# Kernel tuning notes

Hardware: AMD Instinct MI355X
Metric: run time of the kernel (lower is better)

Reference implementation:

```python
import math
import jax, jax.numpy as jnp
import numpy as np
from jax import lax

# Fractional-order LIF constants (Teka et al. style fractional LIF)
ALPHA = 0.2          # fractional order (self.frac_order)
DT = 0.1             # ms
V_L = -70.0          # leak reversal
V_RESET = -70.0      # reset potential
V_TH = -50.0         # spike threshold
G_L = 0.025          # leak conductance
CM = 0.5             # membrane capacitance
KAPPA = (DT ** ALPHA) * math.gamma(2.0 - ALPHA)
EXPO = 1.0 - ALPHA


def _flif_scan(I_seq):
    """Fractional LIF over time. I_seq: [T, B, H] -> (spikes, mems) each [T, B, H].
    V_n = KAPPA * (-G_L*(V_{n-1}-V_L) + I_n)/CM + V_{n-1} - memory_n,
    memory_n = sum_{j=1}^{n-1} c_j * dV_{n-1-j},  c_j = (j+1)^{1-a} - j^{1-a}."""
    T, B, H = I_seq.shape
    dt_f = I_seq.dtype
    j = jnp.arange(T + 1, dtype=jnp.float32)
    c = ((j + 1.0) ** EXPO - j ** EXPO).astype(dt_f)  # c[j], valid for j>=1
    ks = jnp.arange(T)

    def step(carry, xs):
        V, hist = carry            # V: [B,H], hist[k] = dV_k: [T,B,H]
        I, n = xs                  # n = 1..T (1-based step index)
        jidx = n - 1 - ks          # lag j for each history slot k
        w = jnp.where(jidx >= 1, c[jnp.clip(jidx, 0, T)], 0.0)
        memory = jnp.einsum('t,tbh->bh', w, hist)
        f = (-G_L * (V - V_L) + I) / CM
        Vn = KAPPA * f + V - memory
        spk = (Vn >= V_TH).astype(dt_f)
        Vr = jnp.where(spk > 0, V_RESET, Vn)
        hist = hist.at[n - 1].set(Vr - V)
        return (Vr, hist), (spk, Vr)

    V0 = jnp.full((B, H), V_RESET, dtype=dt_f)
    hist0 = jnp.zeros((T, B, H), dtype=dt_f)
    _, (spikes, mems) = lax.scan(step, (V0, hist0), (I_seq, jnp.arange(1, T + 1)))
    return spikes, mems


def setup_inputs() -> dict:
    key = jax.random.key(0)
    k1, k2, k3 = jax.random.split(key, 3)
    B, T, NI, NH, NO = 64, 128, 784, 512, 10
    data = jax.random.uniform(k1, (B, T, NI), dtype=jnp.float32)
    kh = 1.0 / np.sqrt(NI)
    W_h = jnp.abs(jax.random.uniform(k2, (NH, NI), minval=-kh, maxval=kh, dtype=jnp.float32) * 6.0)
    ko = 1.0 / np.sqrt(NH)
    W_o = jnp.abs(jax.random.uniform(k3, (NO, NH), minval=-ko, maxval=ko, dtype=jnp.float32) * 5.0)
    return {"data": data, "W_h": W_h, "W_o": W_o}


def reference(data, W_h, W_o):
    # hidden synapses: [B,T,NI] x [NH,NI] -> [T,B,NH] (time-major for scan)
    I_h = jnp.einsum('btn,hn->tbh', data, W_h)
    spk_h, mem_h = _flif_scan(I_h)
    # output synapses applied per step == one GEMM over all steps
    I_o = jnp.einsum('tbh,oh->tbo', spk_h, W_o)
    spk_o, mem_o = _flif_scan(I_o)
    # matches torch.stack(output_spikes_trace), torch.stack(output_values_trace): [T,B,NO]
    return spk_o, mem_o
```

## Files before the change

### kernel.cpp

```cpp
#include <hip/hip_runtime.h>
#include <hip/hip_bf16.h>
#include <cmath>

#define T_STEPS 128
#define BATCH   64
#define NI      784
#define NIP     800
#define NH      512
#define NO      10
#define M1      (T_STEPS*BATCH)
#define NT_H    (BATCH*NH)
#define NT_O    (BATCH*NO)
#define OUT_HALF (T_STEPS*BATCH*NO)
#define TB      8

typedef __attribute__((ext_vector_type(8))) short short8;
typedef __attribute__((ext_vector_type(4))) float f32x4;
typedef __attribute__((ext_vector_type(8))) unsigned short u16x8;

static __device__ __forceinline__ unsigned short f2b_bits(float x) {
    __hip_bfloat16 h = __float2bfloat16(x);
    return *reinterpret_cast<unsigned short*>(&h);
}
static __device__ __forceinline__ float b2f_bits(unsigned short u) {
    union { unsigned int i; float f; } v; v.i = ((unsigned int)u) << 16; return v.f;
}

template <bool FINAL, int STRIDE>
__device__ __forceinline__ void flif_scan_body(const char* __restrict__ inps,
                                               float* __restrict__ hist,
                                               const float* __restrict__ cs,
                                               void* __restrict__ spikes,
                                               float* __restrict__ mems,
                                               int NT, int nid, int li, float kappa) {
    float cn_[TB];
#pragma unroll
    for (int j = 0; j < TB; ++j) cn_[j] = cs[j];

    float V = -70.f;
    unsigned dvbits = 0u;

    for (int t = 0; t < T_STEPS / TB; ++t) {
        const int n0 = t * TB;

        float Ivv[TB];
#pragma unroll
        for (int i = 0; i < TB; ++i) {
            if constexpr (FINAL) Ivv[i] = ((const float*)inps)[(n0 + i) * STRIDE + li];
            else                 Ivv[i] = __bfloat162float(((const __hip_bfloat16*)inps)[(n0 + i) * STRIDE + li]);
        }
        __builtin_amdgcn_sched_barrier(0);

        float old_[TB];
#pragma unroll
        for (int i = 0; i < TB; ++i) old_[i] = 0.f;

        if (__any(dvbits != 0u)) {
            for (int k0 = 0; k0 < n0; k0 += TB) {
                float hv[TB];
                unsigned sb = 0u;
#pragma unroll
                for (int kk = 0; kk < TB; ++kk) {
                    hv[kk] = hist[(k0 + kk) * STRIDE + li];
                    sb |= __float_as_uint(hv[kk]);
                }
                if (__any(sb != 0u)) {
                    const int base = n0 - k0 - (TB - 1);
                    float cw[2 * TB];
#pragma unroll
                    for (int q = 0; q < 4; ++q) {
                        const float4 cv = *reinterpret_cast<const float4*>(cs + (base - 1) + 4 * q);
                        cw[4 * q + 0] = cv.x; cw[4 * q + 1] = cv.y;
                        cw[4 * q + 2] = cv.z; cw[4 * q + 3] = cv.w;
                    }
#pragma unroll
                    for (int kk = 0; kk < TB; ++kk) {
#pragma unroll
                        for (int i = 0; i < TB; ++i)
                            old_[i] += hv[kk] * cw[TB - kk + i];
                    }
                }
            }
        }

        float dvb[TB];
#pragma unroll
        for (int i = 0; i < TB; ++i) {
            const int nm1 = n0 + i;
            const float Iv = Ivv[i];
            const float f  = (-0.025f * (V + 70.f) + Iv) * 2.0f;
            const float Vn = kappa * f + V - old_[i];
            const bool  sp = (Vn >= -50.f);
            const float Vr = sp ? -70.f : Vn;
            const float dv = Vr - V;
            dvb[i] = dv;
            dvbits |= __float_as_uint(dv);
#pragma unroll
            for (int i2 = i + 1; i2 < TB; ++i2)
                old_[i2] += dv * cn_[i2 - i];
            if (FINAL) {
                ((float*)spikes)[(size_t)nm1 * NT + nid] = sp ? 1.f : 0.f;
                mems[(size_t)nm1 * NT + nid] = Vr;
            } else {
                ((__hip_bfloat16*)spikes)[(size_t)nm1 * NT + nid] = __float2bfloat16(sp ? 1.f : 0.f);
            }
            V = Vr;
        }

        __builtin_amdgcn_sched_barrier(0);
#pragma unroll
        for (int i = 0; i < TB; ++i)
            hist[(n0 + i) * STRIDE + li] = dvb[i];
        __builtin_amdgcn_sched_barrier(0);
    }
}

__global__ __launch_bounds__(256) void prep_kernel(const float* __restrict__ data,
                                                   const float* __restrict__ Wh,
                                                   __hip_bfloat16* __restrict__ Ab,
                                                   __hip_bfloat16* __restrict__ Whb,
                                                   float* __restrict__ ctab) {
    const int bid = blockIdx.x;
    if (bid == 0) {
        const int j = threadIdx.x;
        if (j < 192) {
            double a = pow((double)(j + 1), 0.8);
            double b = pow((double)j, 0.8);
            ctab[j] = (float)(a - b);
        }
        return;
    }
    if (bid <= 6400) {
        const int idx = (bid - 1) * 256 + threadIdx.x;
        const int r  = idx / 200;
        const int n4 = (idx - r * 200) * 4;
        ushort4 o;
        if (n4 < NI) {
            const float4 f = *reinterpret_cast<const float4*>(data + (size_t)r * NI + n4);
            o.x = f2b_bits(f.x); o.y = f2b_bits(f.y); o.z = f2b_bits(f.z); o.w = f2b_bits(f.w);
        } else {
            o.x = o.y = o.z = o.w = 0;
        }
        *reinterpret_cast<ushort4*>(Ab + (size_t)r * NIP + n4) = o;
    } else {
        const int idx = (bid - 6401) * 256 + threadIdx.x;
        const int r  = idx / 200;
        const int n4 = (idx - r * 200) * 4;
        ushort4 o;
        if (n4 < NI) {
            const float4 f = *reinterpret_cast<const float4*>(Wh + (size_t)r * NI + n4);
            o.x = f2b_bits(f.x); o.y = f2b_bits(f.y); o.z = f2b_bits(f.z); o.w = f2b_bits(f.w);
        } else {
            o.x = o.y = o.z = o.w = 0;
        }
        *reinterpret_cast<ushort4*>(Whb + (size_t)r * NIP + n4) = o;
    }
}

__global__ __launch_bounds__(256) void fused1_kernel(const __hip_bfloat16* __restrict__ A,
                                                     const __hip_bfloat16* __restrict__ B,
                                                     __hip_bfloat16* __restrict__ Sh,
                                                     const float* __restrict__ ctab,
                                                     float kappa) {
    __shared__ __hip_bfloat16 As[2][128 * 32];
    __shared__ __hip_bfloat16 Bs[2][64 * 32];
    __shared__ __hip_bfloat16 Ibuf[128 * 64];
    __shared__ float          hist[128 * 64];
    __shared__ __attribute__((aligned(16))) float cs[192];

    const int tid  = threadIdx.x;
    const int wave = tid >> 6, lane = tid & 63;
    const int wm = wave >> 1, wn = wave & 1;
    const int b  = blockIdx.x;
    const int hn = blockIdx.y;
    const int lrow = lane >> 2;
    const int lchk = lane & 3;

    const int NTILES = NIP / 32;

    auto STAGE = [&](int buf, int tt) {
        const int k0 = tt * 32;
#pragma unroll
        for (int p = 0; p < 2; ++p) {
            const int rbase = p * 64 + wave * 16;
            const __hip_bfloat16* g = A + (size_t)(b * T_STEPS + rbase + lrow) * NIP + k0 + lchk * 8;
            __builtin_amdgcn_global_load_lds((const __attribute__((address_space(1))) void*)g,
                                             (__attribute__((address_space(3))) void*)(As[buf] + rbase * 32),
                                             16, 0, 0);
        }
        {
            const __hip_bfloat16* g = B + (size_t)(hn * 64 + wave * 16 + lrow) * NIP + k0 + lchk * 8;
            __builtin_amdgcn_global_load_lds((const __attribute__((address_space(1))) void*)g,
                                             (__attribute__((address_space(3))) void*)(Bs[buf] + wave * 16 * 32),
                                             16, 0, 0);
        }
    };

    f32x4 acc[4][2] = {};

    STAGE(0, 0);
    for (int j = tid; j < 192; j += 256) cs[j] = ctab[j];
    __syncthreads();

    int cur = 0;
    for (int t = 0; t < NTILES; ++t) {
        if (t + 1 < NTILES) STAGE(cur ^ 1, t + 1);

        short8 a[4], bb[2];
#pragma unroll
        for (int i = 0; i < 4; ++i)
            a[i] = *reinterpret_cast<const short8*>(As[cur] + (wm * 64 + i * 16 + (lane & 15)) * 32 + (lane >> 4) * 8);
#pragma unroll
        for (int j = 0; j < 2; ++j)
            bb[j] = *reinterpret_cast<const short8*>(Bs[cur] + (wn * 32 + j * 16 + (lane & 15)) * 32 + (lane >> 4) * 8);
#pragma unroll
        for (int i = 0; i < 4; ++i)
#pragma unroll
            for (int j = 0; j < 2; ++j)
                acc[i][j] = __builtin_amdgcn_mfma_f32_16x16x32_bf16(a[i], bb[j], acc[i][j], 0, 0, 0);

        __syncthreads();
        cur ^= 1;
    }

#pragma unroll
    for (int i = 0; i < 4; ++i) {
#pragma unroll
        for (int j = 0; j < 2; ++j) {
            const int col = wn * 32 + j * 16 + (lane & 15);
#pragma unroll
            for (int r2 = 0; r2 < 4; ++r2) {
                const int row = wm * 64 + i * 16 + (lane >> 4) * 4 + r2;
                Ibuf[row * 64 + col] = __float2bfloat16(acc[i][j][r2]);
            }
        }
    }
    __syncthreads();

    if (tid < 64) {
        flif_scan_body<false, 64>((const char*)Ibuf, hist, cs,
                                  (void*)(Sh + (size_t)b * NH), nullptr,
                                  64 * NH, hn * 64 + tid, tid, kappa);
    }
}

__global__ __launch_bounds__(256) void gemm2_kernel(const __hip_bfloat16* __restrict__ S,
                                                    const float* __restrict__ Wo,
                                                    float* __restrict__ Io) {
    const int wave = threadIdx.x >> 6, lane = threadIdx.x & 63;
    const int r0 = (blockIdx.x * 4 + wave) * 4;

    float wreg[NO][8];
#pragma unroll
    for (int o = 0; o < NO; ++o) {
        const float4 w0 = *reinterpret_cast<const float4*>(Wo + (size_t)o * NH + lane * 8);
        const float4 w1 = *reinterpret_cast<const float4*>(Wo + (size_t)o * NH + lane * 8 + 4);
        wreg[o][0] = w0.x; wreg[o][1] = w0.y; wreg[o][2] = w0.z; wreg[o][3] = w0.w;
        wreg[o][4] = w1.x; wreg[o][5] = w1.y; wreg[o][6] = w1.z; wreg[o][7] = w1.w;
    }

#pragma unroll
    for (int rr = 0; rr < 4; ++rr) {
        const int r = r0 + rr;
        u16x8 raw = *reinterpret_cast<const u16x8*>(S + (size_t)r * NH + lane * 8);
        float s[8];
#pragma unroll
        for (int j = 0; j < 8; ++j) s[j] = b2f_bits(raw[j]);
#pragma unroll
        for (int o = 0; o < NO; ++o) {
            float a = 0.f;
#pragma unroll
            for (int j = 0; j < 8; ++j) a += s[j] * wreg[o][j];
#pragma unroll
            for (int off = 32; off; off >>= 1) a += __shfl_xor(a, off);
            if (lane == o) Io[(size_t)r * NO + o] = a;
        }
    }
}

__global__ __launch_bounds__(64) void flif_final_kernel(const float* __restrict__ Io,
                                                        float* __restrict__ spikes,
                                                        float* __restrict__ mems,
                                                        const float* __restrict__ ctab,
                                                        float kappa) {
    __shared__ float hist[T_STEPS * 64];
    __shared__ __attribute__((aligned(16))) float cs[192];
    __shared__ __attribute__((aligned(16))) char inps[T_STEPS * 64 * 4];
    const int lane = threadIdx.x;
    const int nid  = blockIdx.x * 64 + lane;

#pragma unroll
    for (int q = 0; q < 32; ++q) {
        const float* g = Io +
            ((size_t)(q * 4 + (lane >> 4)) * NT_O + (size_t)blockIdx.x * 64 + (lane & 15) * 4);
        __builtin_amdgcn_global_load_lds((const __attribute__((address_space(1))) void*)g,
                                         (__attribute__((address_space(3))) void*)(inps + q * 1024),
                                         16, 0, 0);
    }
    for (int j = lane; j < 192; j += 64) cs[j] = ctab[j];
    __syncthreads();

    flif_scan_body<true, 64>(inps, hist, cs, spikes, mems, NT_O, nid, lane, kappa);
}

extern "C" void kernel_launch(void* const* d_in, const int* in_sizes, int n_in,
                              void* d_out, int out_size, void* d_ws, size_t ws_size,
                              hipStream_t stream) {
    const float* data = (const float*)d_in[0];
    const float* Wh   = (const float*)d_in[1];
    const float* Wo   = (const float*)d_in[2];
    float* out = (float*)d_out;

    char* ws = (char*)d_ws;
    size_t off = 0;
    auto alloc = [&](size_t bytes) { void* p = ws + off; off += (bytes + 255) & ~255ull; return p; };
    __hip_bfloat16* Ab   = (__hip_bfloat16*)alloc((size_t)M1 * NIP * 2);
    __hip_bfloat16* Whb  = (__hip_bfloat16*)alloc((size_t)NH * NIP * 2);
    __hip_bfloat16* Sh   = (__hip_bfloat16*)alloc((size_t)M1 * NH * 2);
    float*          Io   = (float*)alloc((size_t)M1 * NO * 4);
    float*          ctab = (float*)alloc(192 * 4);

    const float kappa = (float)(std::pow(0.1, 0.2) * std::tgamma(1.8));

    prep_kernel<<<6801, 256, 0, stream>>>(data, Wh, Ab, Whb, ctab);

    dim3 g1(BATCH, NH / 64, 1);
    fused1_kernel<<<g1, 256, 0, stream>>>(Ab, Whb, Sh, ctab, kappa);

    gemm2_kernel<<<M1 / 16, 256, 0, stream>>>(Sh, Wo, Io);

    flif_final_kernel<<<NT_O / 64, 64, 0, stream>>>(Io, out, out + OUT_HALF, ctab, kappa);
}
```

Measured before the change: 65.19 us.

## Deepen GEMM load pipeline to four LDS stages with explicit vmcnt waits

```diff
diff --git a/kernel.cpp b/kernel.cpp
--- a/kernel.cpp
+++ b/kernel.cpp
@@ -162,11 +162,12 @@
                                                      __hip_bfloat16* __restrict__ Sh,
                                                      const float* __restrict__ ctab,
                                                      float kappa) {
-    __shared__ __hip_bfloat16 As[2][128 * 32];
-    __shared__ __hip_bfloat16 Bs[2][64 * 32];
-    __shared__ __hip_bfloat16 Ibuf[128 * 64];
-    __shared__ float          hist[128 * 64];
-    __shared__ __attribute__((aligned(16))) float cs[192];
+    __shared__ __attribute__((aligned(16))) char SMEM[66304];
+    __hip_bfloat16* As   = (__hip_bfloat16*)SMEM;
+    __hip_bfloat16* Bs   = (__hip_bfloat16*)(SMEM + 32768);
+    __hip_bfloat16* Ibuf = (__hip_bfloat16*)(SMEM + 49152);
+    float*          hist = (float*)SMEM;
+    float*          cs   = (float*)(SMEM + 65536);
 
     const int tid  = threadIdx.x;
     const int wave = tid >> 6, lane = tid & 63;
@@ -185,13 +186,13 @@
             const int rbase = p * 64 + wave * 16;
             const __hip_bfloat16* g = A + (size_t)(b * T_STEPS + rbase + lrow) * NIP + k0 + lchk * 8;
             __builtin_amdgcn_global_load_lds((const __attribute__((address_space(1))) void*)g,
-                                             (__attribute__((address_space(3))) void*)(As[buf] + rbase * 32),
+                                             (__attribute__((address_space(3))) void*)(As + buf * (128 * 32) + rbase * 32),
                                              16, 0, 0);
         }
         {
             const __hip_bfloat16* g = B + (size_t)(hn * 64 + wave * 16 + lrow) * NIP + k0 + lchk * 8;
             __builtin_amdgcn_global_load_lds((const __attribute__((address_space(1))) void*)g,
-                                             (__attribute__((address_space(3))) void*)(Bs[buf] + wave * 16 * 32),
+                                             (__attribute__((address_space(3))) void*)(Bs + buf * (64 * 32) + wave * 16 * 32),
                                              16, 0, 0);
         }
     };
@@ -199,28 +200,36 @@
     f32x4 acc[4][2] = {};
 
     STAGE(0, 0);
+    STAGE(1, 1);
+    STAGE(2, 2);
     for (int j = tid; j < 192; j += 256) cs[j] = ctab[j];
     __syncthreads();
 
-    int cur = 0;
     for (int t = 0; t < NTILES; ++t) {
-        if (t + 1 < NTILES) STAGE(cur ^ 1, t + 1);
-
+        if (t + 3 < NTILES) STAGE((t + 3) & 3, t + 3);
+
+        const int cur = t & 3;
         short8 a[4], bb[2];
 #pragma unroll
         for (int i = 0; i < 4; ++i)
-            a[i] = *reinterpret_cast<const short8*>(As[cur] + (wm * 64 + i * 16 + (lane & 15)) * 32 + (lane >> 4) * 8);
+            a[i] = *reinterpret_cast<const short8*>(As + cur * (128 * 32) + (wm * 64 + i * 16 + (lane & 15)) * 32 + (lane >> 4) * 8);
 #pragma unroll
         for (int j = 0; j < 2; ++j)
-            bb[j] = *reinterpret_cast<const short8*>(Bs[cur] + (wn * 32 + j * 16 + (lane & 15)) * 32 + (lane >> 4) * 8);
+            bb[j] = *reinterpret_cast<const short8*>(Bs + cur * (64 * 32) + (wn * 32 + j * 16 + (lane & 15)) * 32 + (lane >> 4) * 8);
 #pragma unroll
         for (int i = 0; i < 4; ++i)
 #pragma unroll
             for (int j = 0; j < 2; ++j)
                 acc[i][j] = __builtin_amdgcn_mfma_f32_16x16x32_bf16(a[i], bb[j], acc[i][j], 0, 0, 0);
 
-        __syncthreads();
-        cur ^= 1;
+        if (t + 1 < NTILES) {
+            if (t <= 21)      asm volatile("s_waitcnt vmcnt(6)" ::: "memory");
+            else if (t == 22) asm volatile("s_waitcnt vmcnt(3)" ::: "memory");
+            else              asm volatile("s_waitcnt vmcnt(0)" ::: "memory");
+            __builtin_amdgcn_sched_barrier(0);
+            __builtin_amdgcn_s_barrier();
+            __builtin_amdgcn_sched_barrier(0);
+        }
     }
 
 #pragma unroll
```

Measured after the change: 57.68 us. -11.5%, faster.
